# Performance work log

Measured on AMD Instinct MI355X. Metric: run time of the kernel, lower is better.

Reference implementation:

```python
import jax, jax.numpy as jnp
import numpy as np

H = 32  # GRU hidden size


def _conv1d(x, w, b, stride, pad):
    # x: (B, Cin, L), w: (Cout, Cin, K)
    y = jax.lax.conv_general_dilated(
        x, w, window_strides=(stride,), padding=[(pad, pad)],
        dimension_numbers=('NCH', 'OIH', 'NCH'))
    return y + b[None, :, None]


def setup_inputs() -> dict:
    key = jax.random.key(0)
    ks = jax.random.split(key, 16)
    B = 16384
    inp = {
        'past_samples': jax.random.normal(ks[0], (B, 2000), jnp.float32),
        'velocity': jax.random.uniform(ks[1], (B,), jnp.float32),
        'log_pitch': jax.random.normal(ks[2], (B,), jnp.float32),
        'time': jax.random.uniform(ks[3], (B,), jnp.float32),
        'hidden_state': jax.random.normal(ks[4], (B, H), jnp.float32),
        # conv stack params
        'w1': jax.random.normal(ks[5], (4, 1, 31), jnp.float32) * 0.1,
        'b1': jnp.zeros((4,), jnp.float32),
        'w2': jax.random.normal(ks[6], (8, 4, 15), jnp.float32) * 0.1,
        'b2': jnp.zeros((8,), jnp.float32),
        'w3': jax.random.normal(ks[7], (16, 8, 7), jnp.float32) * 0.1,
        'b3': jnp.zeros((16,), jnp.float32),
        # GRU params (torch layout: rows = [r; z; n])
        'w_ih': jax.random.normal(ks[8], (3 * H, 19), jnp.float32) * 0.1,
        'w_hh': jax.random.normal(ks[9], (3 * H, H), jnp.float32) * 0.1,
        'b_ih': jnp.zeros((3 * H,), jnp.float32),
        'b_hh': jnp.zeros((3 * H,), jnp.float32),
        # projection
        'w_proj': jax.random.normal(ks[10], (2, H), jnp.float32) * 0.1,
        'b_proj': jnp.zeros((2,), jnp.float32),
    }
    return inp


def reference(past_samples, velocity, log_pitch, time, hidden_state,
              w1, b1, w2, b2, w3, b3, w_ih, w_hh, b_ih, b_hh, w_proj, b_proj):
    x = past_samples[:, None, :]                       # (B,1,2000)
    x = jax.nn.relu(_conv1d(x, w1, b1, 4, 15))         # (B,4,500)
    x = jax.nn.relu(_conv1d(x, w2, b2, 4, 7))          # (B,8,125)
    x = jax.nn.relu(_conv1d(x, w3, b3, 4, 3))          # (B,16,32)
    ctx = jnp.mean(x, axis=2)                          # adaptive avg pool -> (B,16)

    rnn_in = jnp.concatenate(
        [ctx, velocity[:, None], log_pitch[:, None], time[:, None]], axis=1)  # (B,19)

    # single GRU step (torch GRUCell math)
    gi = rnn_in @ w_ih.T + b_ih                        # (B,3H)
    gh = hidden_state @ w_hh.T + b_hh                  # (B,3H)
    r = jax.nn.sigmoid(gi[:, :H] + gh[:, :H])
    z = jax.nn.sigmoid(gi[:, H:2 * H] + gh[:, H:2 * H])
    n = jnp.tanh(gi[:, 2 * H:] + r * gh[:, 2 * H:])
    new_hidden = (1.0 - z) * n + z * hidden_state      # (B,H)

    out = new_hidden @ w_proj.T + b_proj               # (B,2)
    mu, log_sigma = out[:, :1], out[:, 1:]
    sigma = jnp.exp(log_sigma)
    return (mu, sigma, new_hidden)
```

## Files before the change

### kernel.cpp

```cpp
#include <hip/hip_runtime.h>
#include <hip/hip_fp16.h>
#include <math.h>


typedef _Float16 h4 __attribute__((ext_vector_type(4)));
typedef _Float16 h8 __attribute__((ext_vector_type(8)));
typedef float f4 __attribute__((ext_vector_type(4)));

#define PACK_MAG0 0x57A9EDB1u
#define PACK_MAG1 0x1BDE9A75u
#define NITER 8

__device__ __forceinline__ void block_sync_lds()
{
    asm volatile("s_waitcnt lgkmcnt(0)" ::: "memory");
    __builtin_amdgcn_s_barrier();
}
__device__ __forceinline__ void wait_vm0()
{
    asm volatile("s_waitcnt vmcnt(0)" ::: "memory");
}

#if defined(__has_builtin)
#if __has_builtin(__builtin_amdgcn_global_load_lds)
#define HAVE_GLL 1
#endif
#endif

__device__ __forceinline__ void async_ld16(const float* g, float* lds)
{
#ifdef HAVE_GLL
    __builtin_amdgcn_global_load_lds(
        (const __attribute__((address_space(1))) void*)g,
        (__attribute__((address_space(3))) void*)lds, 16, 0, 0);
#else
    const int l = threadIdx.x & 63;
    ((float4*)lds)[l] = ((const float4*)g)[l];
#endif
}

__global__ void pack_weights(const float* __restrict__ w1,
                             const float* __restrict__ w2,
                             const float* __restrict__ w3,
                             const float* __restrict__ w_ih,
                             _Float16* __restrict__ hws,
                             float* __restrict__ wihp,
                             unsigned int* __restrict__ flag)
{
    if (flag[0] == PACK_MAG0 && flag[1] == PACK_MAG1) return;

    for (int i = threadIdx.x; i < 1024; i += 256) {
        int kk = i >> 9, l = (i >> 3) & 63, j = i & 7;
        int m = l & 15, oct = l >> 4;
        int k = kk * 32 + oct * 8 + j;
        int delta = m >> 2, c = m & 3;
        int tap = k - 4 * delta - 1;
        float v = (tap >= 0 && tap < 31) ? w1[c * 31 + tap] : 0.0f;
        hws[i] = (_Float16)v;
    }
    for (int i = threadIdx.x; i < 1024; i += 256) {
        int kk = i >> 9, l = (i >> 3) & 63, j = i & 7;
        int c = l & 15, k = kk * 32 + ((l >> 4) << 3) + j;
        int tap = k >> 2, ci = k & 3;
        float v = (c < 8 && tap < 15) ? w2[(c * 4 + ci) * 15 + tap] : 0.0f;
        hws[1024 + i] = (_Float16)v;
    }
    for (int i = threadIdx.x; i < 1024; i += 256) {
        int kk = i >> 9, l = (i >> 3) & 63, j = i & 7;
        int c = l & 15, k = kk * 32 + ((l >> 4) << 3) + j;
        int tap = k >> 3, ci = k & 7;
        float v = (tap < 7) ? w3[(c * 8 + ci) * 7 + tap] : 0.0f;
        hws[2048 + i] = (_Float16)v;
    }
    for (int idx = threadIdx.x; idx < 96 * 20; idx += 256) {
        int r = idx / 20, c = idx % 20;
        wihp[idx] = (c < 19) ? w_ih[r * 19 + c] : 0.0f;
    }
    __syncthreads();
    if (threadIdx.x == 0) { flag[0] = PACK_MAG0; flag[1] = PACK_MAG1; }
}

__global__ void __launch_bounds__(128, 4)
wavernn_fused(const float* __restrict__ past,
              const float* __restrict__ velocity,
              const float* __restrict__ log_pitch,
              const float* __restrict__ time_in,
              const float* __restrict__ hidden,
              const float* __restrict__ b1,
              const float* __restrict__ b2,
              const float* __restrict__ b3,
              const float* __restrict__ wihp,
              const float* __restrict__ w_hh,
              const float* __restrict__ b_ih, const float* __restrict__ b_hh,
              const float* __restrict__ w_proj, const float* __restrict__ b_proj,
              const _Float16* __restrict__ hws,
              float* __restrict__ out, int B)
{
    __shared__ __align__(16) float    raw[2048];
    __shared__ __align__(16) _Float16 xbuf[2112];
    __shared__ __align__(16) _Float16 y1t[2048];
    __shared__ __align__(16) _Float16 y2t[1056];
    __shared__ float G[192];
    __shared__ float rnnp[2][16];
    __shared__ float hsl[32];
    __shared__ float rnn3[4];

    const h8* const wf1 = (const h8*)hws;
    const h8* const wf2 = (const h8*)(hws + 1024);
    const h8* const wf3 = (const h8*)(hws + 2048);

    const int tid = threadIdx.x;
    const int w   = tid >> 6;
    const int l   = tid & 63;
    const int o   = l >> 4;
    const int q   = l & 15;
    const f4 z4 = {0.0f, 0.0f, 0.0f, 0.0f};

    const int item0 = blockIdx.x * NITER;

    const h8 a10 = wf1[l],      a11 = wf1[64 + l];
    const h8 a20 = wf2[l],      a21 = wf2[64 + l];
    const h8 a30 = wf3[l],      a31 = wf3[64 + l];
    const float bv0 = b1[0], bv1 = b1[1], bv2 = b1[2], bv3 = b1[3];
    float b2v[4], b3v[4];
#pragma unroll
    for (int r = 0; r < 4; ++r) { b2v[r] = b2[(o * 4 + r) & 7];
                                  b3v[r] = b3[o * 4 + r]; }

    if (w == 0) {
        if (l < 16) xbuf[l] = (_Float16)0.0f;
        xbuf[2016 + l] = (_Float16)0.0f;
        if (l < 32) xbuf[2080 + l] = (_Float16)0.0f;
    } else {
        if (l < 28) y1t[l] = (_Float16)0.0f;
        if (l < 20) y1t[2028 + l] = (_Float16)0.0f;
    }
    if (tid < 24) y2t[tid] = (_Float16)0.0f;
    if (tid >= 96) y2t[1024 + (tid - 96)] = (_Float16)0.0f;

    auto stage_issue = [&](int ii) {
        const float* row = past + (size_t)ii * 2000;
#pragma unroll
        for (int c = 0; c < 4; ++c) {
            int foff = w * 1024 + c * 256 + l * 4;
            if (foff > 1996) foff = 1996;
            async_ld16(row + foff, raw + w * 1024 + c * 256);
        }
    };

    stage_issue(item0);

    for (int it = 0; it < NITER; ++it) {
        const int ii = item0 + it;
        if (ii >= B) break;

        wait_vm0();
        if (tid < 32) hsl[tid] = hidden[(size_t)ii * 32 + tid];
        if (tid == 0) { rnn3[0] = velocity[ii];
                        rnn3[1] = log_pitch[ii];
                        rnn3[2] = time_in[ii]; }
        if (tid < 125) {
            const float4* r4 = (const float4*)raw + 4 * tid;
#pragma unroll
            for (int k = 0; k < 4; ++k) {
                float4 v = r4[k];
                h4 hv = {(_Float16)v.x, (_Float16)v.y,
                         (_Float16)v.z, (_Float16)v.w};
                *(h4*)(xbuf + 16 + 16 * tid + 4 * k) = hv;
            }
        }
        block_sync_lds();

        {
            int nx = ii + 1;
            if (nx >= B) nx = B - 1;
            stage_issue(nx);
        }

#pragma unroll
        for (int Ti = 0; Ti < 4; ++Ti) {
            const int T = 4 * w + Ti;
            h8 x0 = *(const h8*)(xbuf + 256 * T + 16 * q + 8 * o);
            h8 x1 = *(const h8*)(xbuf + 256 * T + 16 * q + 32 + 8 * o);
            f4 d = __builtin_amdgcn_mfma_f32_16x16x32_f16(a10, x0, z4, 0, 0, 0);
            d = __builtin_amdgcn_mfma_f32_16x16x32_f16(a11, x1, d, 0, 0, 0);
            const int p = 64 * T + 4 * q + o;
            if (p < 500) {
                h4 wv = {(_Float16)fmaxf(d[0] + bv0, 0.0f),
                         (_Float16)fmaxf(d[1] + bv1, 0.0f),
                         (_Float16)fmaxf(d[2] + bv2, 0.0f),
                         (_Float16)fmaxf(d[3] + bv3, 0.0f)};
                *(h4*)(y1t + (7 + p) * 4) = wv;
            }
        }
        block_sync_lds();

#pragma unroll
        for (int Ti = 0; Ti < 4; ++Ti) {
            const int T = 4 * w + Ti;
            const int p = T * 16 + q;
            h8 x0 = *(const h8*)(y1t + 16 * p + 8 * o);
            h8 x1 = *(const h8*)(y1t + 16 * p + 32 + 8 * o);
            f4 d = __builtin_amdgcn_mfma_f32_16x16x32_f16(a20, x0, z4, 0, 0, 0);
            d = __builtin_amdgcn_mfma_f32_16x16x32_f16(a21, x1, d, 0, 0, 0);
            if (o < 2 && p < 125) {
                h4 wv = {(_Float16)fmaxf(d[0] + b2v[0], 0.0f),
                         (_Float16)fmaxf(d[1] + b2v[1], 0.0f),
                         (_Float16)fmaxf(d[2] + b2v[2], 0.0f),
                         (_Float16)fmaxf(d[3] + b2v[3], 0.0f)};
                *(h4*)(y2t + (3 + p) * 8 + o * 4) = wv;
            }
        }
        block_sync_lds();

        {
            const int p = 16 * w + q;
            h8 x0 = *(const h8*)(y2t + 32 * p + 8 * o);
            h8 x1 = *(const h8*)(y2t + 32 * p + 32 + 8 * o);
            f4 d = __builtin_amdgcn_mfma_f32_16x16x32_f16(a30, x0, z4, 0, 0, 0);
            d = __builtin_amdgcn_mfma_f32_16x16x32_f16(a31, x1, d, 0, 0, 0);
#pragma unroll
            for (int r = 0; r < 4; ++r) {
                float v = fmaxf(d[r] + b3v[r], 0.0f);
                v += __shfl_xor(v, 1); v += __shfl_xor(v, 2);
                v += __shfl_xor(v, 4); v += __shfl_xor(v, 8);
                if (q == 0) rnnp[w][o * 4 + r] = v;
            }
        }
        block_sync_lds();

        if (tid < 96) {
            float rv[20];
#pragma unroll
            for (int j = 0; j < 16; ++j)
                rv[j] = (rnnp[0][j] + rnnp[1][j]) * (1.0f / 32.0f);
            rv[16] = rnn3[0]; rv[17] = rnn3[1]; rv[18] = rnn3[2]; rv[19] = 0.0f;

            float a = b_ih[tid];
            const float4* wr = (const float4*)(wihp + tid * 20);
#pragma unroll
            for (int j = 0; j < 5; ++j) {
                float4 qv = wr[j];
                a += rv[4 * j] * qv.x + rv[4 * j + 1] * qv.y +
                     rv[4 * j + 2] * qv.z + rv[4 * j + 3] * qv.w;
            }
            G[tid] = a;

            float hv[32];
#pragma unroll
            for (int j = 0; j < 32; ++j) hv[j] = hsl[j];

            float g = b_hh[tid];
            const float4* wh = (const float4*)(w_hh + tid * 32);
#pragma unroll
            for (int j = 0; j < 8; ++j) {
                float4 qv = wh[j];
                g += hv[4 * j] * qv.x + hv[4 * j + 1] * qv.y +
                     hv[4 * j + 2] * qv.z + hv[4 * j + 3] * qv.w;
            }
            G[96 + tid] = g;
        }
        block_sync_lds();

        if (tid < 32) {
            const int j = tid;
            float r = 1.0f / (1.0f + expf(-(G[j] + G[96 + j])));
            float z = 1.0f / (1.0f + expf(-(G[32 + j] + G[128 + j])));
            float n = tanhf(G[64 + j] + r * G[160 + j]);
            float nh = (1.0f - z) * n + z * hsl[j];
            out[(size_t)2 * B + (size_t)ii * 32 + j] = nh;

            float p0 = nh * w_proj[j];
            float p1 = nh * w_proj[32 + j];
            p0 += __shfl_xor(p0, 16); p1 += __shfl_xor(p1, 16);
            p0 += __shfl_xor(p0, 8);  p1 += __shfl_xor(p1, 8);
            p0 += __shfl_xor(p0, 4);  p1 += __shfl_xor(p1, 4);
            p0 += __shfl_xor(p0, 2);  p1 += __shfl_xor(p1, 2);
            p0 += __shfl_xor(p0, 1);  p1 += __shfl_xor(p1, 1);
            if (j == 0) {
                out[ii] = p0 + b_proj[0];
                out[B + ii] = expf(p1 + b_proj[1]);
            }
        }
    }
}

extern "C" void kernel_launch(void* const* d_in, const int* in_sizes, int n_in,
                              void* d_out, int out_size, void* d_ws, size_t ws_size,
                              hipStream_t stream)
{
    const float* past      = (const float*)d_in[0];
    const float* velocity  = (const float*)d_in[1];
    const float* log_pitch = (const float*)d_in[2];
    const float* time_in   = (const float*)d_in[3];
    const float* hidden    = (const float*)d_in[4];
    const float* w1  = (const float*)d_in[5];
    const float* b1  = (const float*)d_in[6];
    const float* w2  = (const float*)d_in[7];
    const float* b2  = (const float*)d_in[8];
    const float* w3  = (const float*)d_in[9];
    const float* b3  = (const float*)d_in[10];
    const float* wih = (const float*)d_in[11];
    const float* whh = (const float*)d_in[12];
    const float* bih = (const float*)d_in[13];
    const float* bhh = (const float*)d_in[14];
    const float* wpr = (const float*)d_in[15];
    const float* bpr = (const float*)d_in[16];

    const int B = in_sizes[0] / 2000;
    _Float16* hws = (_Float16*)d_ws;
    float* wihp = (float*)((char*)d_ws + 8192);
    unsigned int* flag = (unsigned int*)((char*)d_ws + 16384);

    pack_weights<<<dim3(1), dim3(256), 0, stream>>>(w1, w2, w3, wih,
                                                    hws, wihp, flag);

    const int nblk = (B + NITER - 1) / NITER;
    wavernn_fused<<<dim3(nblk), dim3(128), 0, stream>>>(
        past, velocity, log_pitch, time_in, hidden,
        b1, b2, b3, wihp, whh, bih, bhh, wpr, bpr,
        (const _Float16*)hws, (float*)d_out, B);
}
```

Baseline: 257.0 us.

## Alias LDS buffers to cut shared memory and raise occupancy

```diff
diff --git a/kernel.cpp b/kernel.cpp
--- a/kernel.cpp
+++ b/kernel.cpp
@@ -9,7 +9,7 @@
 
 #define PACK_MAG0 0x57A9EDB1u
 #define PACK_MAG1 0x1BDE9A75u
-#define NITER 8
+#define NITER 5
 
 __device__ __forceinline__ void block_sync_lds()
 {
@@ -35,7 +35,7 @@
         (__attribute__((address_space(3))) void*)lds, 16, 0, 0);
 #else
     const int l = threadIdx.x & 63;
-    ((float4*)lds)[l] = ((const float4*)g)[l];
+    ((float4*)lds)[l] = *(const float4*)g;
 #endif
 }
 
@@ -80,7 +80,7 @@
     if (threadIdx.x == 0) { flag[0] = PACK_MAG0; flag[1] = PACK_MAG1; }
 }
 
-__global__ void __launch_bounds__(128, 4)
+__global__ void __launch_bounds__(128, 6)
 wavernn_fused(const float* __restrict__ past,
               const float* __restrict__ velocity,
               const float* __restrict__ log_pitch,
@@ -96,14 +96,17 @@
               const _Float16* __restrict__ hws,
               float* __restrict__ out, int B)
 {
-    __shared__ __align__(16) float    raw[2048];
-    __shared__ __align__(16) _Float16 xbuf[2112];
-    __shared__ __align__(16) _Float16 y1t[2048];
-    __shared__ __align__(16) _Float16 y2t[1056];
+    __shared__ __align__(16) float regA[2048];
+    __shared__ __align__(16) _Float16 regB[2112];
     __shared__ float G[192];
     __shared__ float rnnp[2][16];
     __shared__ float hsl[32];
     __shared__ float rnn3[4];
+
+    float* const raw      = regA;
+    _Float16* const y1t   = (_Float16*)regA;
+    _Float16* const xbuf  = regB;
+    _Float16* const y2t   = regB;
 
     const h8* const wf1 = (const h8*)hws;
     const h8* const wf2 = (const h8*)(hws + 1024);
@@ -127,16 +130,7 @@
     for (int r = 0; r < 4; ++r) { b2v[r] = b2[(o * 4 + r) & 7];
                                   b3v[r] = b3[o * 4 + r]; }
 
-    if (w == 0) {
-        if (l < 16) xbuf[l] = (_Float16)0.0f;
-        xbuf[2016 + l] = (_Float16)0.0f;
-        if (l < 32) xbuf[2080 + l] = (_Float16)0.0f;
-    } else {
-        if (l < 28) y1t[l] = (_Float16)0.0f;
-        if (l < 20) y1t[2028 + l] = (_Float16)0.0f;
-    }
-    if (tid < 24) y2t[tid] = (_Float16)0.0f;
-    if (tid >= 96) y2t[1024 + (tid - 96)] = (_Float16)0.0f;
+    if (tid < 96) xbuf[2016 + tid] = (_Float16)0.0f;
 
     auto stage_issue = [&](int ii) {
         const float* row = past + (size_t)ii * 2000;
@@ -159,6 +153,7 @@
         if (tid == 0) { rnn3[0] = velocity[ii];
                         rnn3[1] = log_pitch[ii];
                         rnn3[2] = time_in[ii]; }
+        if (tid < 16) xbuf[tid] = (_Float16)0.0f;
         if (tid < 125) {
             const float4* r4 = (const float4*)raw + 4 * tid;
 #pragma unroll
@@ -171,12 +166,8 @@
         }
         block_sync_lds();
 
-        {
-            int nx = ii + 1;
-            if (nx >= B) nx = B - 1;
-            stage_issue(nx);
-        }
-
+        if (tid < 28) y1t[tid] = (_Float16)0.0f;
+        else if (tid < 48) y1t[2000 + tid] = (_Float16)0.0f;
 #pragma unroll
         for (int Ti = 0; Ti < 4; ++Ti) {
             const int T = 4 * w + Ti;
@@ -195,6 +186,8 @@
         }
         block_sync_lds();
 
+        if (tid < 24) y2t[tid] = (_Float16)0.0f;
+        if (tid >= 96) y2t[928 + tid] = (_Float16)0.0f;
 #pragma unroll
         for (int Ti = 0; Ti < 4; ++Ti) {
             const int T = 4 * w + Ti;
@@ -212,6 +205,8 @@
             }
         }
         block_sync_lds();
+
+        if (it + 1 < NITER && ii + 1 < B) stage_issue(ii + 1);
 
         {
             const int p = 16 * w + q;
```

Result: slower. 388.3 us (+51.1%).
